# Kernel optimization log

Measured on AMD Instinct MI355X. Metric: run time of the kernel, lower is better.

Reference implementation:

```python
import jax, jax.numpy as jnp
import numpy as np

B, S, D = 2, 2048, 1024
H, KS = 16, 64

def setup_inputs() -> dict:
    key = jax.random.key(0)
    k1, k2, k3, k4, k5 = jax.random.split(key, 5)
    return {
        "x": jax.random.normal(k1, (B, S, D), dtype=jnp.float32),
        "Wq": jax.random.normal(k2, (D, KS, H), dtype=jnp.float32) * 0.02,
        "Wk": jax.random.normal(k3, (D, KS, H), dtype=jnp.float32) * 0.02,
        "Wv": jax.random.normal(k4, (D, KS, H), dtype=jnp.float32) * 0.02,
        "kernel": jax.random.normal(k5, (H * KS, KS), dtype=jnp.float32) * 0.02,
    }

def reference(x, Wq, Wk, Wv, kernel):
    b, s, d = x.shape
    ks, h = Wq.shape[1], Wq.shape[2]
    # projections: heads-last layout [b, s, ks, h]
    q = jnp.einsum('bsd,dkh->bskh', x, Wq)
    k = jnp.einsum('bsd,dkh->bskh', x, Wk)
    v = jnp.einsum('bsd,dkh->bskh', x, Wv)
    # scores [b, i(query), l(key), h]
    scores = jnp.einsum('bikh,blkh->bilh', q, k) / jnp.sqrt(jnp.float32(ks))
    # strictly-upper-triangular (future) mask, as in the original:
    # band_part(ones,0,-1) - eye  ->  1 where l > i
    li = jnp.arange(s)
    mask = (li[None, :] > li[:, None]).astype(jnp.float32)  # [s, s]
    scores = scores - 1e8 * mask[None, :, :, None]
    weights = jax.nn.softmax(scores, axis=2)  # softmax over key axis l
    heads = jnp.einsum('bilh,blkh->bikh', weights, v)  # [b, s, ks, h]
    heads = heads.reshape(b, s, ks * h)  # row-major flatten of (ks, h), matching tf.reshape
    return heads @ kernel  # [b, s, ks]
```

## Files before the change

### kernel.cpp

```cpp
#include <hip/hip_runtime.h>
#include <hip/hip_bf16.h>

#define BB 2
#define SS 2048
#define DD 1024
#define HH 16
#define KSZ 64

typedef __attribute__((ext_vector_type(8))) short s16x8;
typedef __attribute__((ext_vector_type(4))) short s16x4;
typedef __attribute__((ext_vector_type(4))) float f32x4;
typedef __attribute__((ext_vector_type(8))) unsigned short u16x8;
typedef __attribute__((ext_vector_type(4))) unsigned short u16x4;
typedef __attribute__((ext_vector_type(2))) unsigned int u32x2;
typedef unsigned short u16;

__device__ __forceinline__ u16 bf16rne(float f) {
  unsigned int u = __float_as_uint(f);
  unsigned int r = (u + 0x7FFFu + ((u >> 16) & 1u)) >> 16;
  return (u16)r;
}

__device__ __forceinline__ unsigned int cvtpk_bf16(float lo, float hi) {
  unsigned int r;
  asm("v_cvt_pk_bf16_f32 %0, %1, %2" : "=v"(r) : "v"(lo), "v"(hi));
  return r;
}

#if __has_builtin(__builtin_amdgcn_mfma_f32_16x16x16_bf16)
__device__ __forceinline__ f32x4 mfma16(s16x4 a, s16x4 b, f32x4 c) {
  return __builtin_amdgcn_mfma_f32_16x16x16_bf16(a, b, c, 0, 0, 0);
}
#elif __has_builtin(__builtin_amdgcn_mfma_f32_16x16x16bf16_1k)
__device__ __forceinline__ f32x4 mfma16(s16x4 a, s16x4 b, f32x4 c) {
  return __builtin_amdgcn_mfma_f32_16x16x16bf16_1k(a, b, c, 0, 0, 0);
}
#else
__device__ __forceinline__ f32x4 mfma16(s16x4 a, s16x4 b, f32x4 c) {
  asm("s_nop 1\n\tv_mfma_f32_16x16x16_bf16 %0, %1, %2, %0"
      : "+v"(c) : "v"(a), "v"(b));
  return c;
}
#endif

__device__ __forceinline__ void lds_dma16(const u16* g, u16* l) {
  __builtin_amdgcn_global_load_lds(
      (const __attribute__((address_space(1))) unsigned int*)(const void*)g,
      (__attribute__((address_space(3))) unsigned int*)(void*)l, 16, 0, 0);
}

__global__ __launch_bounds__(256) void prep_all(
    const float* __restrict__ x, const float* __restrict__ Wq,
    const float* __restrict__ Wk, const float* __restrict__ Wv,
    const float* __restrict__ kern, u16* __restrict__ xb,
    u16* __restrict__ Wt, u16* __restrict__ BpT) {
  __shared__ float Ts[64][65];
  const int bid = blockIdx.x;
  const int tid = threadIdx.x;
  if (bid < 2048) {
    int idx = (bid * 256 + tid) * 8;
    float4 a = *(const float4*)(x + idx);
    float4 b = *(const float4*)(x + idx + 4);
    u16x8 v;
    v[0] = bf16rne(a.x); v[1] = bf16rne(a.y); v[2] = bf16rne(a.z); v[3] = bf16rne(a.w);
    v[4] = bf16rne(b.x); v[5] = bf16rne(b.y); v[6] = bf16rne(b.z); v[7] = bf16rne(b.w);
    *(u16x8*)(xb + idx) = v;
  } else if (bid < 2816) {
    const int bx = bid - 2048;
    const int p = bx >> 8, rem = bx & 255;
    const int d0 = (rem & 15) * 64, n0 = (rem >> 4) * 64;
    const float* W = (p == 0) ? Wq : (p == 1) ? Wk : Wv;
    u16* Wo = Wt + (size_t)p * DD * DD;
    #pragma unroll
    for (int i = 0; i < 4; ++i) {
      int f4 = tid + i * 256;
      int r = f4 >> 4, c4 = f4 & 15;
      float4 v = *(const float4*)(W + (size_t)(d0 + r) * DD + n0 + c4 * 4);
      Ts[r][c4 * 4 + 0] = v.x; Ts[r][c4 * 4 + 1] = v.y;
      Ts[r][c4 * 4 + 2] = v.z; Ts[r][c4 * 4 + 3] = v.w;
    }
    __syncthreads();
    #pragma unroll
    for (int i = 0; i < 4; ++i) {
      int ch = tid + i * 256;
      int n = ch >> 4, d4 = ch & 15;
      u16x4 o;
      #pragma unroll
      for (int j = 0; j < 4; ++j) o[j] = bf16rne(Ts[d4 * 4 + j][n]);
      *(u16x4*)(Wo + (size_t)(n0 + n) * DD + d0 + d4 * 4) = o;
    }
  } else {
    const int n = bid - 2816;
    const int k4 = tid * 4;
    u16x4 o;
    #pragma unroll
    for (int j = 0; j < 4; ++j) {
      int kp = k4 + j;
      int h = kp >> 6, k = kp & 63;
      o[j] = bf16rne(kern[(size_t)(k * HH + h) * KSZ + n]);
    }
    *(u16x4*)(BpT + (size_t)n * (HH * KSZ) + k4) = o;
  }
}

__global__ __launch_bounds__(256) void proj_kernel(
    const u16* __restrict__ xb, const u16* __restrict__ Wt,
    u16* __restrict__ qkvT) {
  const int xcd = blockIdx.x & 7;
  const int idx = blockIdx.x >> 3;
  const int mt = (xcd >> 1) * 8 + (idx & 7);
  const int nt = (xcd & 1) * 4 + ((idx >> 3) & 3);
  const int p  = idx >> 5;
  const int m0 = mt * 128, n0 = nt * 128;
  const u16* W = Wt + (size_t)p * DD * DD;
  u16* outp = qkvT + (size_t)p * (BB * HH * SS * KSZ);

  __shared__ __align__(16) unsigned char raw[49152];
  u16* lds = (u16*)raw;
  u16* Cs  = (u16*)raw;

  const int tid = threadIdx.x;
  const int wave = tid >> 6, lane = tid & 63;
  const int g = lane >> 4, c = lane & 15;
  const int mbase = (wave & 1) * 64, nbase = (wave >> 1) * 64;

  const int lr = lane >> 2, lc = lane & 3;
  const int swz = (lc ^ ((lr >> 1) & 3)) * 8;
  const int rA0 = (wave * 2 + 0) * 16;
  const int rA1 = (wave * 2 + 1) * 16;
  const u16* srcA0 = xb + (size_t)(m0 + rA0 + lr) * DD + swz;
  const u16* srcA1 = xb + (size_t)(m0 + rA1 + lr) * DD + swz;
  const u16* srcB0 = W  + (size_t)(n0 + rA0 + lr) * DD + swz;
  const u16* srcB1 = W  + (size_t)(n0 + rA1 + lr) * DD + swz;
  const int sl0 = rA0 * 32, sl1 = rA1 * 32;

  f32x4 acc[4][4];
  #pragma unroll
  for (int i = 0; i < 4; ++i)
    #pragma unroll
    for (int j = 0; j < 4; ++j) acc[i][j] = {0.f, 0.f, 0.f, 0.f};

  {
    u16* A0 = lds;                u16* B0 = lds + 4096;
    u16* A1 = lds + 8192;         u16* B1 = lds + 8192 + 4096;
    lds_dma16(srcA0, A0 + sl0);       lds_dma16(srcA1, A0 + sl1);
    lds_dma16(srcB0, B0 + sl0);       lds_dma16(srcB1, B0 + sl1);
    lds_dma16(srcA0 + 32, A1 + sl0);  lds_dma16(srcA1 + 32, A1 + sl1);
    lds_dma16(srcB0 + 32, B1 + sl0);  lds_dma16(srcB1 + 32, B1 + sl1);
  }

  const int jsw = (c >> 1) & 3;
  int cr = 0;
  #pragma unroll 1
  for (int t = 0; t < 31; ++t) {
    asm volatile("s_waitcnt vmcnt(4)" ::: "memory");
    __builtin_amdgcn_s_barrier();
    __builtin_amdgcn_sched_barrier(0);
    if (t <= 29) {
      const int st = cr ? cr - 1 : 2;
      const int ko = (t + 2) * 32;
      u16* An = lds + st * 8192;
      u16* Bn = An + 4096;
      lds_dma16(srcA0 + ko, An + sl0);  lds_dma16(srcA1 + ko, An + sl1);
      lds_dma16(srcB0 + ko, Bn + sl0);  lds_dma16(srcB1 + ko, Bn + sl1);
    }
    u16* Ac = lds + cr * 8192;
    u16* Bc = Ac + 4096;
    s16x8 af[4], bfr[4];
    #pragma unroll
    for (int mf = 0; mf < 4; ++mf)
      af[mf] = *(const s16x8*)&Ac[(mbase + mf * 16 + c) * 32 + ((g ^ jsw) * 8)];
    #pragma unroll
    for (int nf = 0; nf < 4; ++nf)
      bfr[nf] = *(const s16x8*)&Bc[(nbase + nf * 16 + c) * 32 + ((g ^ jsw) * 8)];
    #pragma unroll
    for (int mf = 0; mf < 4; ++mf)
      #pragma unroll
      for (int nf = 0; nf < 4; ++nf)
        acc[mf][nf] = __builtin_amdgcn_mfma_f32_16x16x32_bf16(
            af[mf], bfr[nf], acc[mf][nf], 0, 0, 0);
    cr = (cr >= 2) ? 0 : cr + 1;
  }
  asm volatile("s_waitcnt vmcnt(0)" ::: "memory");
  __builtin_amdgcn_s_barrier();
  __builtin_amdgcn_sched_barrier(0);
  {
    u16* Ac = lds + cr * 8192;
    u16* Bc = Ac + 4096;
    s16x8 af[4], bfr[4];
    #pragma unroll
    for (int mf = 0; mf < 4; ++mf)
      af[mf] = *(const s16x8*)&Ac[(mbase + mf * 16 + c) * 32 + ((g ^ jsw) * 8)];
    #pragma unroll
    for (int nf = 0; nf < 4; ++nf)
      bfr[nf] = *(const s16x8*)&Bc[(nbase + nf * 16 + c) * 32 + ((g ^ jsw) * 8)];
    #pragma unroll
    for (int mf = 0; mf < 4; ++mf)
      #pragma unroll
      for (int nf = 0; nf < 4; ++nf)
        acc[mf][nf] = __builtin_amdgcn_mfma_f32_16x16x32_bf16(
            af[mf], bfr[nf], acc[mf][nf], 0, 0, 0);
  }
  __syncthreads();

  const float cscale = (p == 0) ? 0.125f * 1.44269504f : 1.0f;
  #pragma unroll
  for (int mf = 0; mf < 4; ++mf)
    #pragma unroll
    for (int nf = 0; nf < 4; ++nf)
      #pragma unroll
      for (int r = 0; r < 4; ++r)
        Cs[(mbase + mf * 16 + g * 4 + r) * 136 + nbase + nf * 16 + c] =
            bf16rne(acc[mf][nf][r] * cscale);
  __syncthreads();
  const int b = m0 >> 11;
  if (p < 2) {
    int hh = tid >> 4, si = tid & 15;
    #pragma unroll
    for (int i = 0; i < 8; ++i) {
      int row = i * 16 + si;
      int s = (m0 + row) & 2047;
      u16x8 v;
      #pragma unroll
      for (int kp = 0; kp < 8; ++kp) v[kp] = Cs[row * 136 + kp * 16 + hh];
      *(u16x8*)(outp + ((size_t)(b * HH + hh) * SS + s) * KSZ + (n0 >> 4)) = v;
    }
  } else {
    const int s0 = m0 & 2047;
    #pragma unroll
    for (int i = 0; i < 8; ++i) {
      int chunk = tid + i * 256;
      int colid = chunk >> 4;
      int hh = colid >> 3, kp = colid & 7;
      int s8 = chunk & 15;
      u16x8 v;
      #pragma unroll
      for (int j = 0; j < 8; ++j) v[j] = Cs[(s8 * 8 + j) * 136 + kp * 16 + hh];
      *(u16x8*)(outp + ((size_t)(b * HH + hh) * KSZ + (n0 >> 4) + kp) * SS +
                s0 + s8 * 8) = v;
    }
  }
}

__global__ __launch_bounds__(256, 4) void attn_kernel(
    const u16* __restrict__ qkvT, u16* __restrict__ headsB) {
  const int bid = blockIdx.x;
  const int hb = bid & 31;
  const int u  = bid >> 5;
  const int x  = u & 7, w = u >> 3;
  const int it = (w == 0) ? x : (w == 1) ? 15 - x : (w == 2) ? 16 + x : 31 - x;
  const int h = hb & 15, b = hb >> 4;
  const size_t plane = (size_t)(b * HH + h) * SS * KSZ;
  const size_t PSZ = (size_t)BB * HH * SS * KSZ;
  const u16* Qg = qkvT + plane;
  const u16* Kg = qkvT + PSZ + plane;
  const u16* Vg = qkvT + 2 * PSZ + plane;

  __shared__ u16 Ks[2][64 * 64];
  __shared__ u16 Vt[2][64 * 64];

  const int tid = threadIdx.x;
  const int lane = tid & 63;
  const int g = lane >> 4, c = lane & 15;
  const int wq0 = (tid >> 6) * 16;
  const int sr = tid >> 3, sc = tid & 7;
  const int soA = sr * 64 + ((sc ^ (sr & 7)) * 8);
  const int soB = soA + 32 * 64;

  s16x8 bq0 = *(const s16x8*)(Qg + (size_t)(it * 64 + wq0 + c) * KSZ + g * 8);
  s16x8 bq1 = *(const s16x8*)(Qg + (size_t)(it * 64 + wq0 + c) * KSZ + 32 + g * 8);

  u16x8 kr0 = *(const u16x8*)(Kg + (size_t)sr * KSZ + sc * 8);
  u16x8 kr1 = *(const u16x8*)(Kg + (size_t)(sr + 32) * KSZ + sc * 8);
  u16x8 vr0 = *(const u16x8*)(Vg + (size_t)sr * SS + sc * 8);
  u16x8 vr1 = *(const u16x8*)(Vg + (size_t)(sr + 32) * SS + sc * 8);
  *(u16x8*)&Ks[0][soA] = kr0; *(u16x8*)&Ks[0][soB] = kr1;
  *(u16x8*)&Vt[0][soA] = vr0; *(u16x8*)&Vt[0][soB] = vr1;
  kr0 = *(const u16x8*)(Kg + (size_t)(64 + sr) * KSZ + sc * 8);
  kr1 = *(const u16x8*)(Kg + (size_t)(64 + sr + 32) * KSZ + sc * 8);
  vr0 = *(const u16x8*)(Vg + (size_t)sr * SS + 64 + sc * 8);
  vr1 = *(const u16x8*)(Vg + (size_t)(sr + 32) * SS + 64 + sc * 8);
  __syncthreads();

  f32x4 o[4];
  #pragma unroll
  for (int mf = 0; mf < 4; ++mf) o[mf] = {0.f, 0.f, 0.f, 0.f};
  float l_i = 0.f;
  const int cswz = c & 7;
  const int qloc = wq0 + c;

  #pragma unroll 1
  for (int t = 0; t <= it; ++t) {
    const int buf = t & 1;
    if (t < it) {
      const int nb = buf ^ 1;
      *(u16x8*)&Ks[nb][soA] = kr0; *(u16x8*)&Ks[nb][soB] = kr1;
      *(u16x8*)&Vt[nb][soA] = vr0; *(u16x8*)&Vt[nb][soB] = vr1;
      if (t + 2 <= it) {
        const int kv2 = t + 2;
        kr0 = *(const u16x8*)(Kg + (size_t)(kv2 * 64 + sr) * KSZ + sc * 8);
        kr1 = *(const u16x8*)(Kg + (size_t)(kv2 * 64 + sr + 32) * KSZ + sc * 8);
        vr0 = *(const u16x8*)(Vg + (size_t)sr * SS + kv2 * 64 + sc * 8);
        vr1 = *(const u16x8*)(Vg + (size_t)(sr + 32) * SS + kv2 * 64 + sc * 8);
      }
    }
    f32x4 s[4];
    #pragma unroll
    for (int mf = 0; mf < 4; ++mf) s[mf] = {0.f, 0.f, 0.f, 0.f};
    __builtin_amdgcn_s_setprio(1);
    #pragma unroll
    for (int ks = 0; ks < 2; ++ks) {
      const s16x8 bq = ks ? bq1 : bq0;
      #pragma unroll
      for (int mf = 0; mf < 4; ++mf) {
        s16x8 ak = *(const s16x8*)&Ks[buf][(mf * 16 + c) * 64 +
                                          (((ks * 4 + g) ^ cswz) * 8)];
        s[mf] = __builtin_amdgcn_mfma_f32_16x16x32_bf16(ak, bq, s[mf], 0, 0, 0);
      }
    }
    __builtin_amdgcn_s_setprio(0);
    if (t == it) {
      #pragma unroll
      for (int mf = 0; mf < 4; ++mf)
        #pragma unroll
        for (int r = 0; r < 4; ++r)
          if (mf * 16 + g * 4 + r > qloc) s[mf][r] = -1e30f;
    }
    s16x4 bp[4];
    #pragma unroll
    for (int mf = 0; mf < 4; ++mf) {
      float p0 = __builtin_amdgcn_exp2f(s[mf][0]);
      float p1 = __builtin_amdgcn_exp2f(s[mf][1]);
      float p2 = __builtin_amdgcn_exp2f(s[mf][2]);
      float p3 = __builtin_amdgcn_exp2f(s[mf][3]);
      l_i += (p0 + p1) + (p2 + p3);
      u32x2 pk;
      pk[0] = cvtpk_bf16(p0, p1);
      pk[1] = cvtpk_bf16(p2, p3);
      bp[mf] = __builtin_bit_cast(s16x4, pk);
    }
    __builtin_amdgcn_s_setprio(1);
    #pragma unroll
    for (int mf = 0; mf < 4; ++mf) {
      #pragma unroll
      for (int kb = 0; kb < 4; ++kb) {
        s16x4 av = *(const s16x4*)&Vt[buf][(mf * 16 + c) * 64 +
                                           (((kb * 2 + (g >> 1)) ^ cswz) * 8) +
                                           (g & 1) * 4];
        o[mf] = mfma16(av, bp[kb], o[mf]);
      }
    }
    __builtin_amdgcn_s_setprio(0);
    __syncthreads();
  }
  l_i += __shfl_xor(l_i, 16);
  l_i += __shfl_xor(l_i, 32);
  const float inv = 1.0f / l_i;
  const int q = it * 64 + wq0 + c;
  #pragma unroll
  for (int mf = 0; mf < 4; ++mf) {
    u16x4 hv;
    #pragma unroll
    for (int r = 0; r < 4; ++r) hv[r] = bf16rne(o[mf][r] * inv);
    *(u16x4*)(headsB + plane + (size_t)q * KSZ + mf * 16 + g * 4) = hv;
  }
}

__global__ __launch_bounds__(256) void out_kernel(
    const u16* __restrict__ headsB, const u16* __restrict__ BpT,
    float* __restrict__ out) {
  const int m0 = blockIdx.x * 16;
  const int tid = threadIdx.x;
  const int wave = tid >> 6, lane = tid & 63;
  const int g = lane >> 4, c = lane & 15;

  const int m = m0 + c;
  const int b = m >> 11, s = m & 2047;

  f32x4 acc[4];
  #pragma unroll
  for (int nf = 0; nf < 4; ++nf) acc[nf] = {0.f, 0.f, 0.f, 0.f};

  #pragma unroll
  for (int it = 0; it < 8; ++it) {
    const int kb = wave * 256 + it * 32;
    const int hh = kb >> 6, kk = (kb & 63) + g * 8;
    s16x8 a = *(const s16x8*)(headsB +
        ((size_t)(b * HH + hh) * SS + s) * KSZ + kk);
    #pragma unroll
    for (int nf = 0; nf < 4; ++nf) {
      s16x8 bf = *(const s16x8*)(BpT +
          (size_t)(nf * 16 + c) * (HH * KSZ) + kb + g * 8);
      acc[nf] = __builtin_amdgcn_mfma_f32_16x16x32_bf16(a, bf, acc[nf], 0, 0, 0);
    }
  }

  __shared__ __align__(16) float red[4][64][16];
  #pragma unroll
  for (int nf = 0; nf < 4; ++nf)
    *(f32x4*)&red[wave][lane][nf * 4] = acc[nf];
  __syncthreads();

  const int mi = tid >> 4, n4 = (tid & 15) * 4;
  const int gg = mi >> 2, rr = mi & 3;
  float4 res;
  float* rp = &res.x;
  #pragma unroll
  for (int j = 0; j < 4; ++j) {
    int n = n4 + j;
    int cc = n & 15, nf = n >> 4;
    rp[j] = red[0][gg * 16 + cc][nf * 4 + rr] + red[1][gg * 16 + cc][nf * 4 + rr] +
            red[2][gg * 16 + cc][nf * 4 + rr] + red[3][gg * 16 + cc][nf * 4 + rr];
  }
  *(float4*)(out + (size_t)(m0 + mi) * KSZ + n4) = res;
}

extern "C" void kernel_launch(void* const* d_in, const int* in_sizes, int n_in,
                              void* d_out, int out_size, void* d_ws, size_t ws_size,
                              hipStream_t stream) {
  const float* x    = (const float*)d_in[0];
  const float* Wq   = (const float*)d_in[1];
  const float* Wk   = (const float*)d_in[2];
  const float* Wv   = (const float*)d_in[3];
  const float* kern = (const float*)d_in[4];
  float* out = (float*)d_out;

  u16* xb     = (u16*)d_ws;
  u16* Wt     = xb + (size_t)4096 * 1024;
  u16* qkvT   = Wt + (size_t)3 * 1024 * 1024;
  u16* headsB = qkvT + (size_t)3 * BB * HH * SS * KSZ;
  u16* BpT    = headsB + (size_t)BB * HH * SS * KSZ;

  prep_all<<<dim3(2880), 256, 0, stream>>>(x, Wq, Wk, Wv, kern, xb, Wt, BpT);
  proj_kernel<<<dim3(768), 256, 0, stream>>>(xb, Wt, qkvT);
  attn_kernel<<<dim3(1024), 256, 0, stream>>>(qkvT, headsB);
  out_kernel<<<dim3(256), 256, 0, stream>>>(headsB, BpT, out);
}
```

Baseline: 158.3 us.

## Process two KV tiles per barrier step in attention kernel

The attention loop now stages two 64-row K/V tiles per iteration, so each stage holds 128 keys and is double-buffered. This halves the number of __syncthreads and global prefetch rounds per query tile. In exchange it doubles the shared memory footprint (64 KB per block) and register pressure from the extra prefetch registers, and lowers the occupancy hint from 4 to 2 blocks per CU.

```diff
diff --git a/kernel.cpp b/kernel.cpp
--- a/kernel.cpp
+++ b/kernel.cpp
@@ -242,7 +242,7 @@
   }
 }
 
-__global__ __launch_bounds__(256, 4) void attn_kernel(
+__global__ __launch_bounds__(256, 2) void attn_kernel(
     const u16* __restrict__ qkvT, u16* __restrict__ headsB) {
   const int bid = blockIdx.x;
   const int hb = bid & 31;
@@ -256,8 +256,8 @@
   const u16* Kg = qkvT + PSZ + plane;
   const u16* Vg = qkvT + 2 * PSZ + plane;
 
-  __shared__ u16 Ks[2][64 * 64];
-  __shared__ u16 Vt[2][64 * 64];
+  __shared__ u16 Ks[2][2][64 * 64];
+  __shared__ u16 Vt[2][2][64 * 64];
 
   const int tid = threadIdx.x;
   const int lane = tid & 63;
@@ -267,19 +267,38 @@
   const int soA = sr * 64 + ((sc ^ (sr & 7)) * 8);
   const int soB = soA + 32 * 64;
 
+  const int NT = (it >> 1) + 1;
+
   s16x8 bq0 = *(const s16x8*)(Qg + (size_t)(it * 64 + wq0 + c) * KSZ + g * 8);
   s16x8 bq1 = *(const s16x8*)(Qg + (size_t)(it * 64 + wq0 + c) * KSZ + 32 + g * 8);
 
-  u16x8 kr0 = *(const u16x8*)(Kg + (size_t)sr * KSZ + sc * 8);
-  u16x8 kr1 = *(const u16x8*)(Kg + (size_t)(sr + 32) * KSZ + sc * 8);
-  u16x8 vr0 = *(const u16x8*)(Vg + (size_t)sr * SS + sc * 8);
-  u16x8 vr1 = *(const u16x8*)(Vg + (size_t)(sr + 32) * SS + sc * 8);
-  *(u16x8*)&Ks[0][soA] = kr0; *(u16x8*)&Ks[0][soB] = kr1;
-  *(u16x8*)&Vt[0][soA] = vr0; *(u16x8*)&Vt[0][soB] = vr1;
-  kr0 = *(const u16x8*)(Kg + (size_t)(64 + sr) * KSZ + sc * 8);
-  kr1 = *(const u16x8*)(Kg + (size_t)(64 + sr + 32) * KSZ + sc * 8);
-  vr0 = *(const u16x8*)(Vg + (size_t)sr * SS + 64 + sc * 8);
-  vr1 = *(const u16x8*)(Vg + (size_t)(sr + 32) * SS + 64 + sc * 8);
+  const u16* kgA0 = Kg + (size_t)sr * KSZ + sc * 8;
+  const u16* kgA1 = Kg + (size_t)(sr + 32) * KSZ + sc * 8;
+  const u16* vgA0 = Vg + (size_t)sr * SS + sc * 8;
+  const u16* vgA1 = Vg + (size_t)(sr + 32) * SS + sc * 8;
+
+  u16x8 krA0 = *(const u16x8*)(kgA0);
+  u16x8 krA1 = *(const u16x8*)(kgA1);
+  u16x8 krB0 = *(const u16x8*)(kgA0 + (size_t)64 * KSZ);
+  u16x8 krB1 = *(const u16x8*)(kgA1 + (size_t)64 * KSZ);
+  u16x8 vrA0 = *(const u16x8*)(vgA0);
+  u16x8 vrA1 = *(const u16x8*)(vgA1);
+  u16x8 vrB0 = *(const u16x8*)(vgA0 + 64);
+  u16x8 vrB1 = *(const u16x8*)(vgA1 + 64);
+  *(u16x8*)&Ks[0][0][soA] = krA0; *(u16x8*)&Ks[0][0][soB] = krA1;
+  *(u16x8*)&Ks[0][1][soA] = krB0; *(u16x8*)&Ks[0][1][soB] = krB1;
+  *(u16x8*)&Vt[0][0][soA] = vrA0; *(u16x8*)&Vt[0][0][soB] = vrA1;
+  *(u16x8*)&Vt[0][1][soA] = vrB0; *(u16x8*)&Vt[0][1][soB] = vrB1;
+  if (NT > 1) {
+    krA0 = *(const u16x8*)(kgA0 + (size_t)128 * KSZ);
+    krA1 = *(const u16x8*)(kgA1 + (size_t)128 * KSZ);
+    krB0 = *(const u16x8*)(kgA0 + (size_t)192 * KSZ);
+    krB1 = *(const u16x8*)(kgA1 + (size_t)192 * KSZ);
+    vrA0 = *(const u16x8*)(vgA0 + 128);
+    vrA1 = *(const u16x8*)(vgA1 + 128);
+    vrB0 = *(const u16x8*)(vgA0 + 192);
+    vrB1 = *(const u16x8*)(vgA1 + 192);
+  }
   __syncthreads();
 
   f32x4 o[4];
@@ -289,21 +308,7 @@
   const int cswz = c & 7;
   const int qloc = wq0 + c;
 
-  #pragma unroll 1
-  for (int t = 0; t <= it; ++t) {
-    const int buf = t & 1;
-    if (t < it) {
-      const int nb = buf ^ 1;
-      *(u16x8*)&Ks[nb][soA] = kr0; *(u16x8*)&Ks[nb][soB] = kr1;
-      *(u16x8*)&Vt[nb][soA] = vr0; *(u16x8*)&Vt[nb][soB] = vr1;
-      if (t + 2 <= it) {
-        const int kv2 = t + 2;
-        kr0 = *(const u16x8*)(Kg + (size_t)(kv2 * 64 + sr) * KSZ + sc * 8);
-        kr1 = *(const u16x8*)(Kg + (size_t)(kv2 * 64 + sr + 32) * KSZ + sc * 8);
-        vr0 = *(const u16x8*)(Vg + (size_t)sr * SS + kv2 * 64 + sc * 8);
-        vr1 = *(const u16x8*)(Vg + (size_t)(sr + 32) * SS + kv2 * 64 + sc * 8);
-      }
-    }
+  auto do_sub = [&](const u16* Kl, const u16* Vl, bool diag) {
     f32x4 s[4];
     #pragma unroll
     for (int mf = 0; mf < 4; ++mf) s[mf] = {0.f, 0.f, 0.f, 0.f};
@@ -313,13 +318,13 @@
       const s16x8 bq = ks ? bq1 : bq0;
       #pragma unroll
       for (int mf = 0; mf < 4; ++mf) {
-        s16x8 ak = *(const s16x8*)&Ks[buf][(mf * 16 + c) * 64 +
-                                          (((ks * 4 + g) ^ cswz) * 8)];
+        s16x8 ak = *(const s16x8*)&Kl[(mf * 16 + c) * 64 +
+                                      (((ks * 4 + g) ^ cswz) * 8)];
         s[mf] = __builtin_amdgcn_mfma_f32_16x16x32_bf16(ak, bq, s[mf], 0, 0, 0);
       }
     }
     __builtin_amdgcn_s_setprio(0);
-    if (t == it) {
+    if (diag) {
       #pragma unroll
       for (int mf = 0; mf < 4; ++mf)
         #pragma unroll
@@ -344,13 +349,39 @@
     for (int mf = 0; mf < 4; ++mf) {
       #pragma unroll
       for (int kb = 0; kb < 4; ++kb) {
-        s16x4 av = *(const s16x4*)&Vt[buf][(mf * 16 + c) * 64 +
-                                           (((kb * 2 + (g >> 1)) ^ cswz) * 8) +
-                                           (g & 1) * 4];
+        s16x4 av = *(const s16x4*)&Vl[(mf * 16 + c) * 64 +
+                                      (((kb * 2 + (g >> 1)) ^ cswz) * 8) +
+                                      (g & 1) * 4];
         o[mf] = mfma16(av, bp[kb], o[mf]);
       }
     }
     __builtin_amdgcn_s_setprio(0);
+  };
+
+  #pragma unroll 1
+  for (int t = 0; t < NT; ++t) {
+    const int buf = t & 1;
+    if (t + 1 < NT) {
+      const int nb = buf ^ 1;
+      *(u16x8*)&Ks[nb][0][soA] = krA0; *(u16x8*)&Ks[nb][0][soB] = krA1;
+      *(u16x8*)&Ks[nb][1][soA] = krB0; *(u16x8*)&Ks[nb][1][soB] = krB1;
+      *(u16x8*)&Vt[nb][0][soA] = vrA0; *(u16x8*)&Vt[nb][0][soB] = vrA1;
+      *(u16x8*)&Vt[nb][1][soA] = vrB0; *(u16x8*)&Vt[nb][1][soB] = vrB1;
+      if (t + 2 < NT) {
+        const size_t k2 = (size_t)(t + 2) * 128;
+        krA0 = *(const u16x8*)(kgA0 + k2 * KSZ);
+        krA1 = *(const u16x8*)(kgA1 + k2 * KSZ);
+        krB0 = *(const u16x8*)(kgA0 + (k2 + 64) * KSZ);
+        krB1 = *(const u16x8*)(kgA1 + (k2 + 64) * KSZ);
+        vrA0 = *(const u16x8*)(vgA0 + k2);
+        vrA1 = *(const u16x8*)(vgA1 + k2);
+        vrB0 = *(const u16x8*)(vgA0 + k2 + 64);
+        vrB1 = *(const u16x8*)(vgA1 + k2 + 64);
+      }
+    }
+    do_sub(&Ks[buf][0][0], &Vt[buf][0][0], (2 * t) == it);
+    if (2 * t + 1 <= it)
+      do_sub(&Ks[buf][1][0], &Vt[buf][1][0], (2 * t + 1) == it);
     __syncthreads();
   }
   l_i += __shfl_xor(l_i, 16);
```

Result: slower. 163.1 us (+3.1%).
